# Kernel tuning notes

Measured on AMD Instinct MI355X. Metric: run time of the kernel, lower is better.

## Reference

```python
import jax, jax.numpy as jnp
import numpy as np

CODEC_CHANNELS = 8
CODEC_BITS = 10
SOS = 2 ** CODEC_BITS        # 1024
EOS = 2 ** CODEC_BITS + 1    # 1025
PAD = 2 ** CODEC_BITS + 2    # 1026


def setup_inputs() -> dict:
    key = jax.random.key(0)
    k1, k2 = jax.random.split(key)
    B, C, T = 64, CODEC_CHANNELS, 32768
    audio = jax.random.randint(k1, (B, C, T), 0, 1024, dtype=jnp.int64)
    # ragged lengths in [1, T]; force at least one full-length example so the
    # padded output width (max(len)+C) equals T+C as in pad_sequence
    lens = jax.random.randint(k2, (B,), 1, T + 1, dtype=jnp.int64)
    audio_len = lens.at[-1].set(T)
    return {"audio": audio, "audio_len": audio_len, "target": 0}


def reference(audio, audio_len, target):
    # audio: [B, C, T] int, audio_len: [B] int, target: static bool/int
    B, C, T = audio.shape
    offset = 0 if target else 1
    Tout = T + C
    t = jnp.arange(Tout)                     # [Tout]
    start = jnp.arange(C)[:, None] + offset  # [C, 1] per-channel shift
    # source index into the original time axis, clipped for safe gather
    src = jnp.clip(t[None, :] - start, 0, T - 1)          # [C, Tout]
    gathered = jnp.take_along_axis(
        audio, jnp.broadcast_to(src[None], (B, C, Tout)), axis=2
    )                                                      # [B, C, Tout]
    pos = t[None, None, :]                                 # [1, 1, Tout]
    st = start[None]                                       # [1, C, 1]
    ln = audio_len[:, None, None]                          # [B, 1, 1]
    out = jnp.where(pos < st, SOS, gathered)               # leading SOS run
    out = jnp.where(pos >= st + ln, EOS, out)              # trailing EOS run
    out = jnp.where(pos >= ln + C, PAD, out)               # batch padding
    return out, audio_len + C
```

## Files before the change

kernel.cpp:

```cpp
#include <hip/hip_runtime.h>


#define C_CH 8
#define SOS_TOK 1024
#define EOS_TOK 1025
#define PAD_TOK 1026

__global__ __launch_bounds__(256) void delay_audio_kernel(
    const int* __restrict__ audio,
    const int* __restrict__ audio_len,
    const int* __restrict__ target,
    int* __restrict__ out,
    int B, int T, int Tout)
{
    const int chunk = blockIdx.x;
    const int row   = blockIdx.y;
    const int b     = row >> 3;
    const int c     = row & 7;
    const int tid   = threadIdx.x;

    const int offset = (target[0] != 0) ? 0 : 1;
    const int len    = audio_len[b];
    const int start  = c + offset;
    const int eos_at = start + len;
    const int pad_at = len + C_CH;

    const int t0 = chunk << 10;
    const long long arow = (long long)row * T;
    const long long orow = (long long)row * Tout;

    __shared__ __align__(16) int lds[1040];
    const int s0 = t0 - 12;
    {
        int s  = s0 + (tid << 2);
        int sc = min(max(s, 0), T - 4);
        *(int4*)(lds + (tid << 2)) = *(const int4*)(audio + arow + sc);
        if (tid < 4) {
            int i2 = 256 + tid;
            int s2 = s0 + (i2 << 2);
            int sc2 = min(max(s2, 0), T - 4);
            *(int4*)(lds + (i2 << 2)) = *(const int4*)(audio + arow + sc2);
        }
    }
    __syncthreads();

    const int t = t0 + (tid << 2);
    if (t < Tout) {
        const int base = (tid << 2) + 12 - start;
        int v[4];
#pragma unroll
        for (int j = 0; j < 4; ++j) {
            int pos = t + j;
            int g = lds[base + j];
            if (pos < start)   g = SOS_TOK;
            if (pos >= eos_at) g = EOS_TOK;
            if (pos >= pad_at) g = PAD_TOK;
            v[j] = g;
        }
        int4 r; r.x = v[0]; r.y = v[1]; r.z = v[2]; r.w = v[3];
        *(int4*)(out + orow + t) = r;
    }

    if (blockIdx.x == 0 && blockIdx.y == 0 && tid < B) {
        out[(long long)B * C_CH * Tout + tid] = audio_len[tid] + C_CH;
    }
}

extern "C" void kernel_launch(void* const* d_in, const int* in_sizes, int n_in,
                              void* d_out, int out_size, void* d_ws, size_t ws_size,
                              hipStream_t stream) {
    const int* audio     = (const int*)d_in[0];
    const int* audio_len = (const int*)d_in[1];
    const int* target    = (const int*)d_in[2];
    int* out = (int*)d_out;

    const int B = in_sizes[1];
    const int T = in_sizes[0] / (B * C_CH);
    const int Tout = T + C_CH;

    const int chunks = (Tout + 1023) / 1024;
    dim3 grid(chunks, B * C_CH);
    delay_audio_kernel<<<grid, 256, 0, stream>>>(
        audio, audio_len, target, out, B, T, Tout);
}
```

Baseline: 113.5 us.

## Replace LDS staging with direct register vector shifts and nontemporal stores

The shared-memory staging tile and its barrier are removed. Each thread now loads two adjacent int4 words from global memory and builds the shifted output vector in registers using a lane-rotate switch on the per-channel misalignment. Each thread handles two words, so each block covers 2048 elements and half as many blocks are launched. Output goes out through nontemporal stores to avoid polluting the cache. The cost is roughly twice as many global load requests per output word, which are expected to hit in cache, and the code assumes T is a multiple of 4.

After: 110.6 us. 2.5% less time.

```diff
diff --git a/kernel.cpp b/kernel.cpp
--- a/kernel.cpp
+++ b/kernel.cpp
@@ -6,6 +6,8 @@
 #define EOS_TOK 1025
 #define PAD_TOK 1026
 
+typedef int iv4 __attribute__((ext_vector_type(4)));
+
 __global__ __launch_bounds__(256) void delay_audio_kernel(
     const int* __restrict__ audio,
     const int* __restrict__ audio_len,
@@ -13,52 +15,55 @@
     int* __restrict__ out,
     int B, int T, int Tout)
 {
-    const int chunk = blockIdx.x;
-    const int row   = blockIdx.y;
-    const int b     = row >> 3;
-    const int c     = row & 7;
-    const int tid   = threadIdx.x;
+    const int row = blockIdx.y;
+    const int b   = row >> 3;
+    const int c   = row & 7;
+    const int tid = threadIdx.x;
 
     const int offset = (target[0] != 0) ? 0 : 1;
+    const int s      = c + offset;
     const int len    = audio_len[b];
-    const int start  = c + offset;
-    const int eos_at = start + len;
+    const int eos_at = s + len;
     const int pad_at = len + C_CH;
 
-    const int t0 = chunk << 10;
-    const long long arow = (long long)row * T;
-    const long long orow = (long long)row * Tout;
+    const int TW    = T >> 2;
+    const int ToutW = Tout >> 2;
 
-    __shared__ __align__(16) int lds[1040];
-    const int s0 = t0 - 12;
-    {
-        int s  = s0 + (tid << 2);
-        int sc = min(max(s, 0), T - 4);
-        *(int4*)(lds + (tid << 2)) = *(const int4*)(audio + arow + sc);
-        if (tid < 4) {
-            int i2 = 256 + tid;
-            int s2 = s0 + (i2 << 2);
-            int sc2 = min(max(s2, 0), T - 4);
-            *(int4*)(lds + (i2 << 2)) = *(const int4*)(audio + arow + sc2);
+    const int qw = (s + 3) >> 2;
+    const int d  = (4 - (s & 3)) & 3;
+
+    const iv4* aw = (const iv4*)audio + (long long)row * TW;
+    iv4*       ow = (iv4*)out + (long long)row * ToutW;
+
+    const int baseW = blockIdx.x << 9;
+
+#pragma unroll
+    for (int h = 0; h < 2; ++h) {
+        const int W = baseW + (h << 8) + tid;
+        if (W >= ToutW) continue;
+        const int wa  = W - qw;
+        const int wai = min(max(wa, 0),     TW - 1);
+        const int wbi = min(max(wa + 1, 0), TW - 1);
+        const iv4 A  = aw[wai];
+        const iv4 Bv = aw[wbi];
+
+        iv4 g;
+        switch (d) {
+            case 0:  g = A; break;
+            case 1:  g = (iv4){A.y, A.z, A.w, Bv.x}; break;
+            case 2:  g = (iv4){A.z, A.w, Bv.x, Bv.y}; break;
+            default: g = (iv4){A.w, Bv.x, Bv.y, Bv.z}; break;
         }
-    }
-    __syncthreads();
 
-    const int t = t0 + (tid << 2);
-    if (t < Tout) {
-        const int base = (tid << 2) + 12 - start;
-        int v[4];
+        const int t = W << 2;
 #pragma unroll
         for (int j = 0; j < 4; ++j) {
-            int pos = t + j;
-            int g = lds[base + j];
-            if (pos < start)   g = SOS_TOK;
-            if (pos >= eos_at) g = EOS_TOK;
-            if (pos >= pad_at) g = PAD_TOK;
-            v[j] = g;
+            const int pos = t + j;
+            if (pos < s)       g[j] = SOS_TOK;
+            if (pos >= eos_at) g[j] = EOS_TOK;
+            if (pos >= pad_at) g[j] = PAD_TOK;
         }
-        int4 r; r.x = v[0]; r.y = v[1]; r.z = v[2]; r.w = v[3];
-        *(int4*)(out + orow + t) = r;
+        __builtin_nontemporal_store(g, &ow[W]);
     }
 
     if (blockIdx.x == 0 && blockIdx.y == 0 && tid < B) {
@@ -78,7 +83,8 @@
     const int T = in_sizes[0] / (B * C_CH);
     const int Tout = T + C_CH;
 
-    const int chunks = (Tout + 1023) / 1024;
+    const int ToutW  = Tout >> 2;
+    const int chunks = (ToutW + 511) / 512;
     dim3 grid(chunks, B * C_CH);
     delay_audio_kernel<<<grid, 256, 0, stream>>>(
         audio, audio_len, target, out, B, T, Tout);
```
